# Performance work log

Hardware: AMD Instinct MI355X
Metric: run time of the kernel (lower is better)

The kernel has to match this reference:

```python
import jax, jax.numpy as jnp
import numpy as np

B, N, D, H = 16384, 64, 64, 128
DECAY_W = 2.0  # Decayer(2, 'rev') -> 1 / (1 + w * dt)
EPS = 1e-12


def setup_inputs() -> dict:
    key = jax.random.key(0)
    ks = jax.random.split(key, 16)
    return {
        "dt_node": jax.random.uniform(ks[0], (B,)) * 10.0,
        "deg_node": jax.random.uniform(ks[1], (B,)),
        "cc_node": jax.random.uniform(ks[2], (B,)),
        "dt_neigh": jax.random.uniform(ks[3], (B, N)) * 10.0,
        "deg_neigh": jax.random.uniform(ks[4], (B, N)),
        "cc_neigh": jax.random.uniform(ks[5], (B, N)),
        "neigh_mask": jax.random.bernoulli(ks[6], 0.7, (B, N)),
        "feature_hist": jax.random.normal(ks[7], (B, 2 * D)),
        "t2v_w": jax.random.normal(ks[8], (D,)) * 0.1,
        "t2v_b": jax.random.normal(ks[9], (D,)) * 0.1,
        "node_w": jax.random.normal(ks[10], (D,)) * 0.1,
        "node_b": jax.random.normal(ks[11], (D,)) * 0.1,
        "att_W1": jax.random.normal(ks[12], (D, D)) * (1.0 / np.sqrt(D)),
        "att_W2": jax.random.normal(ks[13], (D, D)) * (1.0 / np.sqrt(D)),
        "att_v": jax.random.normal(ks[14], (D,)) * (1.0 / np.sqrt(D)),
        "weight": jax.random.normal(ks[15], (H, 4 * D)) * (1.0 / np.sqrt(4 * D)),
    }


def _time2vec(t, w, b):
    # Time2Vec('cos'): first channel linear, rest cos-activated. t: [...], -> [..., D]
    v = t[..., None] * w + b
    return jnp.concatenate([v[..., :1], jnp.cos(v[..., 1:])], axis=-1)


def _node_feat(dt, deg, cc, t2v_w, t2v_b, node_w, node_b):
    # linear_node(deg) + linear_node(cc) + time2vec(|dt|), then L2 normalize
    f = (_time2vec(jnp.abs(dt), t2v_w, t2v_b)
         + (deg[..., None] * node_w + node_b)
         + (cc[..., None] * node_w + node_b))
    nrm = jnp.maximum(jnp.linalg.norm(f, axis=-1, keepdims=True), EPS)
    return f / nrm


def reference(dt_node, deg_node, cc_node, dt_neigh, deg_neigh, cc_neigh,
              neigh_mask, feature_hist, t2v_w, t2v_b, node_w, node_b,
              att_W1, att_W2, att_v, weight):
    node_f = _node_feat(dt_node, deg_node, cc_node, t2v_w, t2v_b, node_w, node_b)      # [B, D]
    neigh_f = _node_feat(dt_neigh, deg_neigh, cc_neigh, t2v_w, t2v_b, node_w, node_b)  # [B, N, D]

    # temporal decay: Decayer(2, 'rev')
    time_score = 1.0 / (1.0 + DECAY_W * dt_neigh)                                       # [B, N]

    h = jnp.tanh((node_f @ att_W1)[:, None, :] + jnp.einsum('bnd,de->bne', neigh_f, att_W2))
    att = jnp.einsum('bne,e->bn', h, att_v)                                             # [B, N]

    score = jax.nn.leaky_relu(time_score) * att                                         # [B, N]
    m = neigh_mask.astype(node_f.dtype)
    n_in = jnp.maximum(jnp.sum(m, axis=-1, keepdims=True), 1.0)                         # [B, 1]
    w_n = (m * score) / n_in                                                            # [B, N]
    neigh_agg = jnp.einsum('bn,bnd->bd', w_n, neigh_f)                                  # [B, D]

    combined = jnp.concatenate([node_f, neigh_agg, feature_hist], axis=-1)              # [B, 4D]
    return jax.nn.relu(combined @ weight.T)                                             # [B, H]
```

## Files before the change

kernel.cpp:

```cpp
#include <hip/hip_runtime.h>
#include <hip/hip_bf16.h>

#define B_SZ 16384
#define N_SZ 64
#define D_SZ 64
#define H_SZ 128
#define R_PB 4
#define ARS 72
#define CRS 264

typedef short bf16x8 __attribute__((ext_vector_type(8)));
typedef float f32x4  __attribute__((ext_vector_type(4)));

__device__ __forceinline__ float bflo(unsigned u){union{unsigned i;float f;}c;c.i=u<<16;return c.f;}
__device__ __forceinline__ float bfhi(unsigned u){union{unsigned i;float f;}c;c.i=u&0xffff0000u;return c.f;}
__device__ __forceinline__ float bits2f(unsigned short r){union{unsigned i;float f;}c;c.i=((unsigned)r)<<16;return c.f;}
__device__ __forceinline__ unsigned f2bfbits(float f){
    __hip_bfloat16 h = __float2bfloat16(f);
    return (unsigned)__builtin_bit_cast(unsigned short, h);
}
__device__ __forceinline__ float bf2f(__hip_bfloat16 x) { return __bfloat162float(x); }

template<int CTRL>
__device__ __forceinline__ float dpp_add(float v){
    int t = __builtin_amdgcn_mov_dpp(__builtin_bit_cast(int, v), CTRL, 0xf, 0xf, true);
    return v + __builtin_bit_cast(float, t);
}

__device__ __forceinline__ float tanh_fast(float x){
    float e = __expf(2.0f * x);
    return 1.0f - __fdividef(2.0f, e + 1.0f);
}

template<int FMODE>
__device__ __forceinline__ float LD(const void* p, int i) {
    if constexpr (FMODE == 0) return bf2f(((const __hip_bfloat16*)p)[i]);
    else                      return ((const float*)p)[i];
}

template<int FMODE>
__device__ __forceinline__ void load16(const void* p, int off, float* o) {
    if constexpr (FMODE == 0) {
        const uint4* q = (const uint4*)((const unsigned short*)p + off);
        uint4 a = q[0], b = q[1];
        o[0]=bflo(a.x); o[1]=bfhi(a.x); o[2]=bflo(a.y); o[3]=bfhi(a.y);
        o[4]=bflo(a.z); o[5]=bfhi(a.z); o[6]=bflo(a.w); o[7]=bfhi(a.w);
        o[8]=bflo(b.x); o[9]=bfhi(b.x); o[10]=bflo(b.y); o[11]=bfhi(b.y);
        o[12]=bflo(b.z); o[13]=bfhi(b.z); o[14]=bflo(b.w); o[15]=bfhi(b.w);
    } else {
        const float4* q = (const float4*)((const float*)p + off);
        float4 a=q[0],b=q[1],c=q[2],d=q[3];
        o[0]=a.x;o[1]=a.y;o[2]=a.z;o[3]=a.w; o[4]=b.x;o[5]=b.y;o[6]=b.z;o[7]=b.w;
        o[8]=c.x;o[9]=c.y;o[10]=c.z;o[11]=c.w; o[12]=d.x;o[13]=d.y;o[14]=d.z;o[15]=d.w;
    }
}

__device__ __forceinline__ float mval(const void* p, int i, int mode) {
    if (mode == 0) return ((const int*)p)[i]            ? 1.0f : 0.0f;
    if (mode == 1) return ((const unsigned char*)p)[i]  ? 1.0f : 0.0f;
    if (mode == 2) return ((const unsigned short*)p)[i] ? 1.0f : 0.0f;
    return ((const unsigned int*)p)[i]                  ? 1.0f : 0.0f;
}

__device__ int detect_f32(const void* p) {
    const unsigned short* u = (const unsigned short*)p;
    unsigned any_hi = 0;
    for (int i = 0; i < 64; ++i) any_hi |= (u[i] & 0x8000u);
    return any_hi ? 1 : 0;
}

__device__ int detect_mask_mode(const void* p) {
    const unsigned char* u = (const unsigned char*)p;
    unsigned o0 = 0, o1 = 0, o2 = 0, o3 = 0, vmax = 0;
    for (int i = 0; i < 128; i += 4) {
        unsigned a = u[i], b = u[i + 1], c = u[i + 2], d = u[i + 3];
        o0 |= a; o1 |= b; o2 |= c; o3 |= d;
        unsigned m1 = a > b ? a : b, m2 = c > d ? c : d;
        unsigned m = m1 > m2 ? m1 : m2;
        vmax = vmax > m ? vmax : m;
    }
    if ((o1 | o2 | o3) == 0) return 0;
    if (vmax <= 1)           return 1;
    if (o0 > 1)              return 2;
    return 3;
}

__global__ void prep_kernel(const void* dt_node, const void* att_W1, const void* att_W2,
                            void* ws) {
    const int tid   = threadIdx.x;
    const int fmode = detect_f32(dt_node);
    #pragma unroll
    for (int it = 0; it < 4; ++it) {
        const int t   = tid + it * 256;
        const int fi  = t >> 6, ln = t & 63;
        const int et  = fi >> 2, ks = fi & 3;
        const int m16 = ln & 15, qd = ln >> 4;
        const int col = et * 16 + m16;
        unsigned short s[8];
        #pragma unroll
        for (int j = 0; j < 8; ++j) {
            const int i = ks * 32 + qd * 8 + j;
            if (fmode == 0) {
                s[j] = (i < 64) ? ((const unsigned short*)att_W1)[i * D_SZ + col]
                                : ((const unsigned short*)att_W2)[(i - 64) * D_SZ + col];
            } else {
                const float v = (i < 64) ? ((const float*)att_W1)[i * D_SZ + col]
                                         : ((const float*)att_W2)[(i - 64) * D_SZ + col];
                s[j] = (unsigned short)f2bfbits(v);
            }
        }
        uint4 v = make_uint4(((unsigned)s[0]) | (((unsigned)s[1]) << 16),
                             ((unsigned)s[2]) | (((unsigned)s[3]) << 16),
                             ((unsigned)s[4]) | (((unsigned)s[5]) << 16),
                             ((unsigned)s[6]) | (((unsigned)s[7]) << 16));
        ((uint4*)ws)[t] = v;
    }
}

struct Smem {
    alignas(16) unsigned short A[R_PB * 65 * ARS];
    alignas(16) unsigned short comb[R_PB * CRS];
    float att[R_PB][N_SZ];
    float wn[R_PB][N_SZ];
    int modes[2];
};

template<int FMODE>
__device__ __forceinline__ void feat_row(float t, float dc,
                                         const float* w16, const float* b16_,
                                         const float* nw16, const float* nb16,
                                         int c, unsigned short* dstA, unsigned short* dstC) {
    float f[16]; float ss = 0.0f;
    #pragma unroll
    for (int j = 0; j < 16; ++j) {
        float v  = fmaf(t, w16[j], b16_[j]);
        float tv = (c == 0 && j == 0) ? v : __cosf(v);
        f[j] = tv + fmaf(dc, nw16[j], 2.0f * nb16[j]);
        ss = fmaf(f[j], f[j], ss);
    }
    ss += __shfl_xor(ss, 1, 4);
    ss += __shfl_xor(ss, 2, 4);
    const float inv = 1.0f / fmaxf(sqrtf(ss), 1e-12f);
    unsigned pk[8];
    #pragma unroll
    for (int j = 0; j < 8; ++j)
        pk[j] = f2bfbits(f[2*j] * inv) | (f2bfbits(f[2*j+1] * inv) << 16);
    uint4 v0 = make_uint4(pk[0], pk[1], pk[2], pk[3]);
    uint4 v1 = make_uint4(pk[4], pk[5], pk[6], pk[7]);
    ((uint4*)dstA)[0] = v0; ((uint4*)dstA)[1] = v1;
    if (dstC) { ((uint4*)dstC)[0] = v0; ((uint4*)dstC)[1] = v1; }
}

template<int FMODE, bool USE_WS>
__device__ __forceinline__ void body(
    Smem& sm,
    const void* dt_node, const void* deg_node, const void* cc_node,
    const void* dt_neigh, const void* deg_neigh, const void* cc_neigh,
    const void* neigh_mask, const void* feature_hist,
    const void* t2v_w, const void* t2v_b, const void* node_w, const void* node_b,
    const void* att_W1, const void* att_W2, const void* att_v,
    const void* weight, void* out, const void* ws, int mmode, int b0, int tid)
{
    const int lane = tid & 63;
    const int wv   = tid >> 6;
    const int m16  = lane & 15;
    const int quad = lane >> 4;

    #pragma unroll
    for (int it = 0; it < 5; ++it) {
        const int t = tid + it * 256;
        if (t < R_PB * 65 * 4) {
            const int f = t >> 2, c = t & 3, d0 = c * 16;
            float w16[16], b16_[16], nw16[16], nb16[16];
            load16<FMODE>(t2v_w,  d0, w16);
            load16<FMODE>(t2v_b,  d0, b16_);
            load16<FMODE>(node_w, d0, nw16);
            load16<FMODE>(node_b, d0, nb16);
            if (f < R_PB * 64) {
                const int row = f >> 6, n = f & 63;
                const int idx = (b0 + row) * N_SZ + n;
                const float tn  = fabsf(LD<FMODE>(dt_neigh, idx));
                const float dcn = LD<FMODE>(deg_neigh, idx) + LD<FMODE>(cc_neigh, idx);
                feat_row<FMODE>(tn, dcn, w16, b16_, nw16, nb16, c,
                                sm.A + (row * 65 + n) * ARS + d0, nullptr);
            } else {
                const int row = f - R_PB * 64;
                const float tn = fabsf(LD<FMODE>(dt_node, b0 + row));
                const float dc = LD<FMODE>(deg_node, b0 + row) + LD<FMODE>(cc_node, b0 + row);
                feat_row<FMODE>(tn, dc, w16, b16_, nw16, nb16, c,
                                sm.A + (row * 65 + 64) * ARS + d0,
                                sm.comb + row * CRS + d0);
            }
        }
    }
    __syncthreads();

    {
        const int r = wv;
        const unsigned short* An = sm.A + (r * 65 + 64) * ARS + quad * 8;
        const bf16x8 a0 = *(const bf16x8*)An;
        const bf16x8 a1 = *(const bf16x8*)(An + 32);
        const bf16x8* wfrag = (const bf16x8*)ws;

        f32x4  accN[4];
        bf16x8 w2f[4], w3f[4];
        float  ve[4];
        #pragma unroll
        for (int et = 0; et < 4; ++et) {
            bf16x8 w0, w1;
            if constexpr (USE_WS) {
                w0      = wfrag[(et * 4 + 0) * 64 + lane];
                w1      = wfrag[(et * 4 + 1) * 64 + lane];
                w2f[et] = wfrag[(et * 4 + 2) * 64 + lane];
                w3f[et] = wfrag[(et * 4 + 3) * 64 + lane];
            } else {
                const int col = et * 16 + m16;
                #pragma unroll
                for (int j = 0; j < 8; ++j) {
                    const int k0 = quad * 8 + j;
                    if constexpr (FMODE == 0) {
                        w0[j]      = (short)((const unsigned short*)att_W1)[k0 * D_SZ + col];
                        w1[j]      = (short)((const unsigned short*)att_W1)[(k0 + 32) * D_SZ + col];
                        w2f[et][j] = (short)((const unsigned short*)att_W2)[k0 * D_SZ + col];
                        w3f[et][j] = (short)((const unsigned short*)att_W2)[(k0 + 32) * D_SZ + col];
                    } else {
                        w0[j]      = (short)f2bfbits(((const float*)att_W1)[k0 * D_SZ + col]);
                        w1[j]      = (short)f2bfbits(((const float*)att_W1)[(k0 + 32) * D_SZ + col]);
                        w2f[et][j] = (short)f2bfbits(((const float*)att_W2)[k0 * D_SZ + col]);
                        w3f[et][j] = (short)f2bfbits(((const float*)att_W2)[(k0 + 32) * D_SZ + col]);
                    }
                }
            }
            f32x4 z = {0.f, 0.f, 0.f, 0.f};
            z = __builtin_amdgcn_mfma_f32_16x16x32_bf16(a0, w0, z, 0, 0, 0);
            z = __builtin_amdgcn_mfma_f32_16x16x32_bf16(a1, w1, z, 0, 0, 0);
            accN[et] = z;
            ve[et]   = LD<FMODE>(att_v, et * 16 + m16);
        }

        #pragma unroll
        for (int mt = 0; mt < 4; ++mt) {
            const unsigned short* Ar = sm.A + (r * 65 + mt * 16 + m16) * ARS + quad * 8;
            const bf16x8 a2 = *(const bf16x8*)Ar;
            const bf16x8 a3 = *(const bf16x8*)(Ar + 32);
            float p0 = 0.f, p1 = 0.f, p2 = 0.f, p3 = 0.f;
            #pragma unroll
            for (int et = 0; et < 4; ++et) {
                f32x4 acc = __builtin_amdgcn_mfma_f32_16x16x32_bf16(a2, w2f[et], accN[et], 0, 0, 0);
                acc       = __builtin_amdgcn_mfma_f32_16x16x32_bf16(a3, w3f[et], acc,      0, 0, 0);
                p0 = fmaf(tanh_fast(acc[0]), ve[et], p0);
                p1 = fmaf(tanh_fast(acc[1]), ve[et], p1);
                p2 = fmaf(tanh_fast(acc[2]), ve[et], p2);
                p3 = fmaf(tanh_fast(acc[3]), ve[et], p3);
            }
            p0 = dpp_add<0xB1>(p0); p0 = dpp_add<0x4E>(p0); p0 = dpp_add<0x124>(p0); p0 = dpp_add<0x128>(p0);
            p1 = dpp_add<0xB1>(p1); p1 = dpp_add<0x4E>(p1); p1 = dpp_add<0x124>(p1); p1 = dpp_add<0x128>(p1);
            p2 = dpp_add<0xB1>(p2); p2 = dpp_add<0x4E>(p2); p2 = dpp_add<0x124>(p2); p2 = dpp_add<0x128>(p2);
            p3 = dpp_add<0xB1>(p3); p3 = dpp_add<0x4E>(p3); p3 = dpp_add<0x124>(p3); p3 = dpp_add<0x128>(p3);
            if (m16 == 0) {
                sm.att[r][mt * 16 + quad * 4 + 0] = p0;
                sm.att[r][mt * 16 + quad * 4 + 1] = p1;
                sm.att[r][mt * 16 + quad * 4 + 2] = p2;
                sm.att[r][mt * 16 + quad * 4 + 3] = p3;
            }
        }
    }

    {
        const int r   = wv;
        const int idx = (b0 + r) * N_SZ + lane;
        const float dt = LD<FMODE>(dt_neigh, idx);
        const float ts = 1.0f / fmaf(2.0f, dt, 1.0f);
        const float lr = ts >= 0.0f ? ts : 0.01f * ts;
        const float m  = mval(neigh_mask, idx, mmode);
        float cnt = m;
        #pragma unroll
        for (int off = 32; off > 0; off >>= 1) cnt += __shfl_down(cnt, off, 64);
        cnt = __shfl(cnt, 0, 64);
        sm.wn[r][lane] = m * lr * sm.att[r][lane] / fmaxf(cnt, 1.0f);

        if constexpr (FMODE == 0) {
            const unsigned u = ((const unsigned*)feature_hist)[(b0 + r) * 64 + lane];
            *(unsigned*)(sm.comb + r * CRS + 2 * D_SZ + 2 * lane) = u;
        } else {
            const float* fh = (const float*)feature_hist + (b0 + r) * 2 * D_SZ + 2 * lane;
            *(unsigned*)(sm.comb + r * CRS + 2 * D_SZ + 2 * lane) =
                f2bfbits(fh[0]) | (f2bfbits(fh[1]) << 16);
        }
    }

    {
        const int r = wv;
        float agg = 0.0f;
        #pragma unroll
        for (int n = 0; n < N_SZ; ++n) {
            const float w = sm.wn[r][n];
            agg = fmaf(w, bits2f(sm.A[(r * 65 + n) * ARS + lane]), agg);
        }
        sm.comb[r * CRS + D_SZ + lane] = (unsigned short)f2bfbits(agg);
    }
    __syncthreads();

    {
        #pragma unroll
        for (int t2 = 0; t2 < 2; ++t2) {
            const int nt = wv * 2 + t2;
            f32x4 c = {0.f, 0.f, 0.f, 0.f};
            #pragma unroll
            for (int ks = 0; ks < 8; ++ks) {
                const bf16x8 af = *(const bf16x8*)(sm.comb + (m16 & 3) * CRS + ks * 32 + quad * 8);
                bf16x8 bw;
                if constexpr (FMODE == 0) {
                    bw = *(const bf16x8*)((const unsigned short*)weight
                            + (nt * 16 + m16) * (4 * D_SZ) + ks * 32 + quad * 8);
                } else {
                    const float* wr = (const float*)weight
                            + (nt * 16 + m16) * (4 * D_SZ) + ks * 32 + quad * 8;
                    #pragma unroll
                    for (int j = 0; j < 8; ++j) bw[j] = (short)f2bfbits(wr[j]);
                }
                c = __builtin_amdgcn_mfma_f32_16x16x32_bf16(af, bw, c, 0, 0, 0);
            }
            if (quad == 0) {
                #pragma unroll
                for (int rr = 0; rr < 4; ++rr) {
                    const float v = fmaxf(c[rr], 0.0f);
                    if constexpr (FMODE == 0)
                        ((__hip_bfloat16*)out)[(b0 + rr) * H_SZ + nt * 16 + m16] = __float2bfloat16(v);
                    else
                        ((float*)out)[(b0 + rr) * H_SZ + nt * 16 + m16] = v;
                }
            }
        }
    }
}

template<bool USE_WS>
__global__ __launch_bounds__(256, 3) void fused_model_kernel(
    const void* dt_node, const void* deg_node, const void* cc_node,
    const void* dt_neigh, const void* deg_neigh, const void* cc_neigh,
    const void* neigh_mask, const void* feature_hist,
    const void* t2v_w, const void* t2v_b, const void* node_w, const void* node_b,
    const void* att_W1, const void* att_W2, const void* att_v,
    const void* weight, void* out, const void* ws)
{
    __shared__ Smem sm;
    const int b0  = blockIdx.x * R_PB;
    const int tid = threadIdx.x;

    if (tid == 0) {
        sm.modes[0] = detect_f32(dt_node);
        sm.modes[1] = detect_mask_mode(neigh_mask);
    }
    __syncthreads();
    const int fmode = __builtin_amdgcn_readfirstlane(sm.modes[0]);
    const int mmode = __builtin_amdgcn_readfirstlane(sm.modes[1]);

    if (fmode == 0)
        body<0, USE_WS>(sm, dt_node, deg_node, cc_node, dt_neigh, deg_neigh, cc_neigh,
                        neigh_mask, feature_hist, t2v_w, t2v_b, node_w, node_b,
                        att_W1, att_W2, att_v, weight, out, ws, mmode, b0, tid);
    else
        body<1, USE_WS>(sm, dt_node, deg_node, cc_node, dt_neigh, deg_neigh, cc_neigh,
                        neigh_mask, feature_hist, t2v_w, t2v_b, node_w, node_b,
                        att_W1, att_W2, att_v, weight, out, ws, mmode, b0, tid);
}

extern "C" void kernel_launch(void* const* d_in, const int* in_sizes, int n_in,
                              void* d_out, int out_size, void* d_ws, size_t ws_size,
                              hipStream_t stream) {
    const bool use_ws = (ws_size >= 16384) && (d_ws != nullptr);
    if (use_ws) {
        prep_kernel<<<1, 256, 0, stream>>>(d_in[0], d_in[12], d_in[13], d_ws);
        fused_model_kernel<true><<<B_SZ / R_PB, 256, 0, stream>>>(
            d_in[0], d_in[1], d_in[2], d_in[3], d_in[4], d_in[5], d_in[6], d_in[7],
            d_in[8], d_in[9], d_in[10], d_in[11], d_in[12], d_in[13], d_in[14], d_in[15],
            d_out, d_ws);
    } else {
        fused_model_kernel<false><<<B_SZ / R_PB, 256, 0, stream>>>(
            d_in[0], d_in[1], d_in[2], d_in[3], d_in[4], d_in[5], d_in[6], d_in[7],
            d_in[8], d_in[9], d_in[10], d_in[11], d_in[12], d_in[13], d_in[14], d_in[15],
            d_out, d_ws);
    }
}
```

Baseline: 243.3 us.

## Vectorize format detection, hoist parameter loads, pack bf16 pairs, raise occupancy

```diff
diff --git a/kernel.cpp b/kernel.cpp
--- a/kernel.cpp
+++ b/kernel.cpp
@@ -6,7 +6,7 @@
 #define D_SZ 64
 #define H_SZ 128
 #define R_PB 4
-#define ARS 72
+#define ARS 68
 #define CRS 264
 
 typedef short bf16x8 __attribute__((ext_vector_type(8)));
@@ -17,7 +17,15 @@
 __device__ __forceinline__ float bits2f(unsigned short r){union{unsigned i;float f;}c;c.i=((unsigned)r)<<16;return c.f;}
 __device__ __forceinline__ unsigned f2bfbits(float f){
     __hip_bfloat16 h = __float2bfloat16(f);
-    return (unsigned)__builtin_bit_cast(unsigned short, h);
+    unsigned short u;
+    __builtin_memcpy(&u, &h, 2);
+    return (unsigned)u;
+}
+__device__ __forceinline__ unsigned pack2bf(float a, float b){
+    __hip_bfloat162 h = __float22bfloat162_rn(make_float2(a, b));
+    unsigned r;
+    __builtin_memcpy(&r, &h, 4);
+    return r;
 }
 __device__ __forceinline__ float bf2f(__hip_bfloat16 x) { return __bfloat162float(x); }
 
@@ -62,59 +70,55 @@
     return ((const unsigned int*)p)[i]                  ? 1.0f : 0.0f;
 }
 
-__device__ int detect_f32(const void* p) {
-    const unsigned short* u = (const unsigned short*)p;
-    unsigned any_hi = 0;
-    for (int i = 0; i < 64; ++i) any_hi |= (u[i] & 0x8000u);
-    return any_hi ? 1 : 0;
-}
-
-__device__ int detect_mask_mode(const void* p) {
-    const unsigned char* u = (const unsigned char*)p;
-    unsigned o0 = 0, o1 = 0, o2 = 0, o3 = 0, vmax = 0;
-    for (int i = 0; i < 128; i += 4) {
-        unsigned a = u[i], b = u[i + 1], c = u[i + 2], d = u[i + 3];
-        o0 |= a; o1 |= b; o2 |= c; o3 |= d;
-        unsigned m1 = a > b ? a : b, m2 = c > d ? c : d;
-        unsigned m = m1 > m2 ? m1 : m2;
-        vmax = vmax > m ? vmax : m;
-    }
-    if ((o1 | o2 | o3) == 0) return 0;
-    if (vmax <= 1)           return 1;
-    if (o0 > 1)              return 2;
+__device__ __forceinline__ int detect_f32(const void* p) {
+    const uint4* q = (const uint4*)p;
+    unsigned o = 0;
+    #pragma unroll
+    for (int i = 0; i < 8; ++i) { uint4 v = q[i]; o |= v.x | v.y | v.z | v.w; }
+    return (o & 0x80008000u) ? 1 : 0;
+}
+
+__device__ __forceinline__ int detect_mask_mode(const void* p) {
+    const uint4* q = (const uint4*)p;
+    unsigned oa = 0, ofe = 0;
+    #pragma unroll
+    for (int i = 0; i < 8; ++i) {
+        uint4 v = q[i];
+        unsigned w = v.x | v.y | v.z | v.w;
+        oa  |= w;
+        ofe |= (v.x & 0xFEFEFEFEu) | (v.y & 0xFEFEFEFEu) | (v.z & 0xFEFEFEFEu) | (v.w & 0xFEFEFEFEu);
+    }
+    if ((oa & 0xFFFFFF00u) == 0) return 0;
+    if (ofe == 0)                return 1;
+    if (oa & 0x000000FEu)        return 2;
     return 3;
 }
 
 __global__ void prep_kernel(const void* dt_node, const void* att_W1, const void* att_W2,
                             void* ws) {
-    const int tid   = threadIdx.x;
+    const int t     = blockIdx.x * 256 + threadIdx.x;
     const int fmode = detect_f32(dt_node);
-    #pragma unroll
-    for (int it = 0; it < 4; ++it) {
-        const int t   = tid + it * 256;
-        const int fi  = t >> 6, ln = t & 63;
-        const int et  = fi >> 2, ks = fi & 3;
-        const int m16 = ln & 15, qd = ln >> 4;
-        const int col = et * 16 + m16;
-        unsigned short s[8];
-        #pragma unroll
-        for (int j = 0; j < 8; ++j) {
-            const int i = ks * 32 + qd * 8 + j;
-            if (fmode == 0) {
-                s[j] = (i < 64) ? ((const unsigned short*)att_W1)[i * D_SZ + col]
-                                : ((const unsigned short*)att_W2)[(i - 64) * D_SZ + col];
-            } else {
-                const float v = (i < 64) ? ((const float*)att_W1)[i * D_SZ + col]
-                                         : ((const float*)att_W2)[(i - 64) * D_SZ + col];
-                s[j] = (unsigned short)f2bfbits(v);
-            }
-        }
-        uint4 v = make_uint4(((unsigned)s[0]) | (((unsigned)s[1]) << 16),
-                             ((unsigned)s[2]) | (((unsigned)s[3]) << 16),
-                             ((unsigned)s[4]) | (((unsigned)s[5]) << 16),
-                             ((unsigned)s[6]) | (((unsigned)s[7]) << 16));
-        ((uint4*)ws)[t] = v;
-    }
+    const int fi  = t >> 6, ln = t & 63;
+    const int et  = fi >> 2, ks = fi & 3;
+    const int m16 = ln & 15, qd = ln >> 4;
+    const int col = et * 16 + m16;
+    unsigned short s[8];
+    #pragma unroll
+    for (int j = 0; j < 8; ++j) {
+        const int i = ks * 32 + qd * 8 + j;
+        if (fmode == 0) {
+            s[j] = (i < 64) ? ((const unsigned short*)att_W1)[i * D_SZ + col]
+                            : ((const unsigned short*)att_W2)[(i - 64) * D_SZ + col];
+        } else {
+            const float v = (i < 64) ? ((const float*)att_W1)[i * D_SZ + col]
+                                     : ((const float*)att_W2)[(i - 64) * D_SZ + col];
+            s[j] = (unsigned short)f2bfbits(v);
+        }
+    }
+    ((uint4*)ws)[t] = make_uint4(((unsigned)s[0]) | (((unsigned)s[1]) << 16),
+                                 ((unsigned)s[2]) | (((unsigned)s[3]) << 16),
+                                 ((unsigned)s[4]) | (((unsigned)s[5]) << 16),
+                                 ((unsigned)s[6]) | (((unsigned)s[7]) << 16));
 }
 
 struct Smem {
@@ -122,7 +126,6 @@
     alignas(16) unsigned short comb[R_PB * CRS];
     float att[R_PB][N_SZ];
     float wn[R_PB][N_SZ];
-    int modes[2];
 };
 
 template<int FMODE>
@@ -135,7 +138,7 @@
     for (int j = 0; j < 16; ++j) {
         float v  = fmaf(t, w16[j], b16_[j]);
         float tv = (c == 0 && j == 0) ? v : __cosf(v);
-        f[j] = tv + fmaf(dc, nw16[j], 2.0f * nb16[j]);
+        f[j] = tv + fmaf(dc, nw16[j], nb16[j]);
         ss = fmaf(f[j], f[j], ss);
     }
     ss += __shfl_xor(ss, 1, 4);
@@ -144,7 +147,7 @@
     unsigned pk[8];
     #pragma unroll
     for (int j = 0; j < 8; ++j)
-        pk[j] = f2bfbits(f[2*j] * inv) | (f2bfbits(f[2*j+1] * inv) << 16);
+        pk[j] = pack2bf(f[2*j] * inv, f[2*j+1] * inv);
     uint4 v0 = make_uint4(pk[0], pk[1], pk[2], pk[3]);
     uint4 v1 = make_uint4(pk[4], pk[5], pk[6], pk[7]);
     ((uint4*)dstA)[0] = v0; ((uint4*)dstA)[1] = v1;
@@ -166,30 +169,36 @@
     const int m16  = lane & 15;
     const int quad = lane >> 4;
 
-    #pragma unroll
-    for (int it = 0; it < 5; ++it) {
-        const int t = tid + it * 256;
-        if (t < R_PB * 65 * 4) {
-            const int f = t >> 2, c = t & 3, d0 = c * 16;
-            float w16[16], b16_[16], nw16[16], nb16[16];
-            load16<FMODE>(t2v_w,  d0, w16);
-            load16<FMODE>(t2v_b,  d0, b16_);
-            load16<FMODE>(node_w, d0, nw16);
-            load16<FMODE>(node_b, d0, nb16);
-            if (f < R_PB * 64) {
-                const int row = f >> 6, n = f & 63;
-                const int idx = (b0 + row) * N_SZ + n;
-                const float tn  = fabsf(LD<FMODE>(dt_neigh, idx));
-                const float dcn = LD<FMODE>(deg_neigh, idx) + LD<FMODE>(cc_neigh, idx);
-                feat_row<FMODE>(tn, dcn, w16, b16_, nw16, nb16, c,
-                                sm.A + (row * 65 + n) * ARS + d0, nullptr);
-            } else {
-                const int row = f - R_PB * 64;
-                const float tn = fabsf(LD<FMODE>(dt_node, b0 + row));
-                const float dc = LD<FMODE>(deg_node, b0 + row) + LD<FMODE>(cc_node, b0 + row);
-                feat_row<FMODE>(tn, dc, w16, b16_, nw16, nb16, c,
-                                sm.A + (row * 65 + 64) * ARS + d0,
-                                sm.comb + row * CRS + d0);
+    {
+        const int c = tid & 3, d0 = c * 16;
+        float w16[16], b16_[16], nw16[16], nb16[16];
+        load16<FMODE>(t2v_w,  d0, w16);
+        load16<FMODE>(t2v_b,  d0, b16_);
+        load16<FMODE>(node_w, d0, nw16);
+        load16<FMODE>(node_b, d0, nb16);
+        #pragma unroll
+        for (int j = 0; j < 16; ++j) nb16[j] *= 2.0f;
+
+        #pragma unroll
+        for (int it = 0; it < 5; ++it) {
+            const int t = tid + it * 256;
+            if (t < R_PB * 65 * 4) {
+                const int f = t >> 2;
+                if (f < R_PB * 64) {
+                    const int row = f >> 6, n = f & 63;
+                    const int idx = (b0 + row) * N_SZ + n;
+                    const float tn  = fabsf(LD<FMODE>(dt_neigh, idx));
+                    const float dcn = LD<FMODE>(deg_neigh, idx) + LD<FMODE>(cc_neigh, idx);
+                    feat_row<FMODE>(tn, dcn, w16, b16_, nw16, nb16, c,
+                                    sm.A + (row * 65 + n) * ARS + d0, nullptr);
+                } else {
+                    const int row = f - R_PB * 64;
+                    const float tn = fabsf(LD<FMODE>(dt_node, b0 + row));
+                    const float dc = LD<FMODE>(deg_node, b0 + row) + LD<FMODE>(cc_node, b0 + row);
+                    feat_row<FMODE>(tn, dc, w16, b16_, nw16, nb16, c,
+                                    sm.A + (row * 65 + 64) * ARS + d0,
+                                    sm.comb + row * CRS + d0);
+                }
             }
         }
     }
@@ -284,8 +293,7 @@
             *(unsigned*)(sm.comb + r * CRS + 2 * D_SZ + 2 * lane) = u;
         } else {
             const float* fh = (const float*)feature_hist + (b0 + r) * 2 * D_SZ + 2 * lane;
-            *(unsigned*)(sm.comb + r * CRS + 2 * D_SZ + 2 * lane) =
-                f2bfbits(fh[0]) | (f2bfbits(fh[1]) << 16);
+            *(unsigned*)(sm.comb + r * CRS + 2 * D_SZ + 2 * lane) = pack2bf(fh[0], fh[1]);
         }
     }
 
@@ -336,7 +344,7 @@
 }
 
 template<bool USE_WS>
-__global__ __launch_bounds__(256, 3) void fused_model_kernel(
+__global__ __launch_bounds__(256, 4) void fused_model_kernel(
     const void* dt_node, const void* deg_node, const void* cc_node,
     const void* dt_neigh, const void* deg_neigh, const void* cc_neigh,
     const void* neigh_mask, const void* feature_hist,
@@ -348,13 +356,8 @@
     const int b0  = blockIdx.x * R_PB;
     const int tid = threadIdx.x;
 
-    if (tid == 0) {
-        sm.modes[0] = detect_f32(dt_node);
-        sm.modes[1] = detect_mask_mode(neigh_mask);
-    }
-    __syncthreads();
-    const int fmode = __builtin_amdgcn_readfirstlane(sm.modes[0]);
-    const int mmode = __builtin_amdgcn_readfirstlane(sm.modes[1]);
+    const int fmode = __builtin_amdgcn_readfirstlane(detect_f32(dt_node));
+    const int mmode = __builtin_amdgcn_readfirstlane(detect_mask_mode(neigh_mask));
 
     if (fmode == 0)
         body<0, USE_WS>(sm, dt_node, deg_node, cc_node, dt_neigh, deg_neigh, cc_neigh,
@@ -371,7 +374,7 @@
                               hipStream_t stream) {
     const bool use_ws = (ws_size >= 16384) && (d_ws != nullptr);
     if (use_ws) {
-        prep_kernel<<<1, 256, 0, stream>>>(d_in[0], d_in[12], d_in[13], d_ws);
+        prep_kernel<<<4, 256, 0, stream>>>(d_in[0], d_in[12], d_in[13], d_ws);
         fused_model_kernel<true><<<B_SZ / R_PB, 256, 0, stream>>>(
             d_in[0], d_in[1], d_in[2], d_in[3], d_in[4], d_in[5], d_in[6], d_in[7],
             d_in[8], d_in[9], d_in[10], d_in[11], d_in[12], d_in[13], d_in[14], d_in[15],
```

After: 218.5 us. -10.2%, faster.
